# Performance work log

Hardware: AMD Instinct MI355X
Metric: run time of the kernel (lower is better)

Reference implementation:

```python
import jax, jax.numpy as jnp
import numpy as np

# Static config (matches init_kwargs)
B, H, W, C = 8, 80, 60, 512
WS, SHIFT = 10, 5
NH = 16
HD = C // NH  # 32
L = WS * WS  # 100 tokens per window
NW = (H // WS) * (W // WS)  # 48 windows per image
EPS = 1e-5


def _relative_position_index():
    coords = np.stack(np.meshgrid(np.arange(WS), np.arange(WS), indexing='ij'))  # (2,WS,WS)
    flat = coords.reshape(2, -1)  # (2, L)
    rel = flat[:, :, None] - flat[:, None, :]  # (2, L, L)
    rel = rel.transpose(1, 2, 0)  # (L, L, 2)
    rel[:, :, 0] += WS - 1
    rel[:, :, 1] += WS - 1
    rel[:, :, 0] *= 2 * WS - 1
    return rel.sum(-1)  # (L, L) indices into (2*WS-1)^2 table


def _attn_mask():
    # Swin shift mask: label 3x3 regions, tokens in different regions cannot attend.
    img = np.zeros((H, W), dtype=np.float32)
    slices = (slice(0, -WS), slice(-WS, -SHIFT), slice(-SHIFT, None))
    cnt = 0
    for hs in slices:
        for ws_ in slices:
            img[hs, ws_] = cnt
            cnt += 1
    mw = img.reshape(H // WS, WS, W // WS, WS).transpose(0, 2, 1, 3).reshape(NW, L)
    diff = mw[:, None, :] - mw[:, :, None]  # (NW, L, L)
    return np.where(diff != 0, -100.0, 0.0).astype(np.float32)


REL_IDX = jnp.asarray(_relative_position_index())
ATTN_MASK = jnp.asarray(_attn_mask())


def layernorm(x, g, b):
    mu = jnp.mean(x, axis=-1, keepdims=True)
    var = jnp.mean(jnp.square(x - mu), axis=-1, keepdims=True)
    return (x - mu) * jax.lax.rsqrt(var + EPS) * g + b


def setup_inputs() -> dict:
    key = jax.random.key(0)
    ks = jax.random.split(key, 8)
    s = 0.02
    return {
        'hidden_states': jax.random.normal(ks[0], (B, H * W, C), jnp.float32),
        'ln1_g': jnp.ones((C,), jnp.float32),
        'ln1_b': jnp.zeros((C,), jnp.float32),
        'wq': jax.random.normal(ks[1], (C, C), jnp.float32) * s,
        'bq': jnp.zeros((C,), jnp.float32),
        'wk': jax.random.normal(ks[2], (C, C), jnp.float32) * s,
        'bk': jnp.zeros((C,), jnp.float32),
        'wv': jax.random.normal(ks[3], (C, C), jnp.float32) * s,
        'bv': jnp.zeros((C,), jnp.float32),
        'wo': jax.random.normal(ks[4], (C, C), jnp.float32) * s,
        'bo': jnp.zeros((C,), jnp.float32),
        'rel_bias_table': jax.random.normal(ks[5], ((2 * WS - 1) ** 2, NH), jnp.float32) * s,
        'ln2_g': jnp.ones((C,), jnp.float32),
        'ln2_b': jnp.zeros((C,), jnp.float32),
        'w1': jax.random.normal(ks[6], (C, 4 * C), jnp.float32) * s,
        'b1': jnp.zeros((4 * C,), jnp.float32),
        'w2': jax.random.normal(ks[7], (4 * C, C), jnp.float32) * s,
        'b2': jnp.zeros((C,), jnp.float32),
    }


def reference(hidden_states, ln1_g, ln1_b, wq, bq, wk, bk, wv, bv, wo, bo,
              rel_bias_table, ln2_g, ln2_b, w1, b1, w2, b2):
    shortcut = hidden_states  # (B, H*W, C)
    x = layernorm(hidden_states, ln1_g, ln1_b).reshape(B, H, W, C)
    # cyclic shift (H, W divisible by WS -> no padding needed)
    x = jnp.roll(x, (-SHIFT, -SHIFT), axis=(1, 2))
    # window partition -> (B*NW, L, C)
    win = x.reshape(B, H // WS, WS, W // WS, WS, C).transpose(0, 1, 3, 2, 4, 5)
    win = win.reshape(B * NW, L, C)
    # multi-head attention within windows
    q = (win @ wq + bq).reshape(-1, L, NH, HD).transpose(0, 2, 1, 3)
    k = (win @ wk + bk).reshape(-1, L, NH, HD).transpose(0, 2, 1, 3)
    v = (win @ wv + bv).reshape(-1, L, NH, HD).transpose(0, 2, 1, 3)
    scores = jnp.einsum('bhqd,bhkd->bhqk', q, k) / np.sqrt(HD).astype(np.float32)
    bias = rel_bias_table[REL_IDX.reshape(-1)].reshape(L, L, NH).transpose(2, 0, 1)
    scores = scores + bias[None]  # (B*NW, NH, L, L)
    scores = scores.reshape(B, NW, NH, L, L) + ATTN_MASK[None, :, None]
    attn = jax.nn.softmax(scores.reshape(B * NW, NH, L, L), axis=-1)
    ctx = jnp.einsum('bhqk,bhkd->bhqd', attn, v).transpose(0, 2, 1, 3).reshape(B * NW, L, C)
    out = ctx @ wo + bo
    # window reverse + un-shift
    out = out.reshape(B, H // WS, W // WS, WS, WS, C).transpose(0, 1, 3, 2, 4, 5)
    out = out.reshape(B, H, W, C)
    out = jnp.roll(out, (SHIFT, SHIFT), axis=(1, 2)).reshape(B, H * W, C)
    hs = shortcut + out
    # FFN with post-residual layernorm input
    y = layernorm(hs, ln2_g, ln2_b)
    y = jax.nn.gelu(y @ w1 + b1, approximate=False) @ w2 + b2
    return hs + y
```

## Files before the change

kernel.cpp:

```cpp
#include <hip/hip_runtime.h>
#include <math.h>

typedef unsigned short u16;
typedef unsigned int u32;
typedef __bf16 bf16x8 __attribute__((ext_vector_type(8)));
typedef float f32x4 __attribute__((ext_vector_type(4)));

__device__ __forceinline__ float b2f(u16 u) { return __uint_as_float(((u32)u) << 16); }
__device__ __forceinline__ u16 f2b(float f) {
    u32 x = __float_as_uint(f);
    return (u16)((x + 0x7FFFu + ((x >> 16) & 1u)) >> 16);
}
__device__ __forceinline__ void load8f(const float* p, size_t idx, float* o) {
    const float4* q = (const float4*)(p + idx);
    float4 a = q[0], b = q[1];
    o[0]=a.x; o[1]=a.y; o[2]=a.z; o[3]=a.w; o[4]=b.x; o[5]=b.y; o[6]=b.z; o[7]=b.w;
}
__device__ __forceinline__ void gld16(const void* g, void* l) {
    __builtin_amdgcn_global_load_lds(
        (const __attribute__((address_space(1))) u32*)g,
        (__attribute__((address_space(3))) u32*)l, 16, 0, 0);
}

__global__ __launch_bounds__(256) void transpose_k(const float* __restrict__ Win, u16* __restrict__ Wt,
                                                   int Kd, int Nd, float scale) {
    __shared__ u16 tile[32][33];
    int tx = threadIdx.x & 31, ty = threadIdx.x >> 5;
    int k0 = blockIdx.x << 5, n0 = blockIdx.y << 5;
#pragma unroll
    for (int r = 0; r < 4; r++)
        tile[ty + 8 * r][tx] = f2b(Win[(size_t)(k0 + ty + 8 * r) * Nd + (n0 + tx)] * scale);
    __syncthreads();
#pragma unroll
    for (int r = 0; r < 4; r++)
        Wt[(size_t)(n0 + ty + 8 * r) * Kd + (k0 + tx)] = tile[tx][ty + 8 * r];
}

__global__ __launch_bounds__(256) void biascat_k(const float* __restrict__ bq, const float* __restrict__ bk,
                                                 const float* __restrict__ bv, float* __restrict__ o) {
    int i = blockIdx.x * 256 + threadIdx.x;
    float v = (i < 512) ? bq[i] * 0.17677669529663689f : (i < 1024 ? bk[i - 512] : bv[i - 1024]);
    o[i] = v;
}

__global__ __launch_bounds__(256) void ln1win_k(const float* __restrict__ x, const float* __restrict__ g,
                                                const float* __restrict__ bta, u16* __restrict__ win) {
    int wave = threadIdx.x >> 6, lane = threadIdx.x & 63;
    int token = blockIdx.x * 4 + wave;
    int b = token / 4800, rem = token - b * 4800;
    int h = rem / 60, w = rem - h * 60;
    int hr = h + 75; if (hr >= 80) hr -= 80;
    int wr = w + 55; if (wr >= 60) wr -= 60;
    int widx = (hr / 10) * 6 + (wr / 10);
    int l = (hr - (hr / 10) * 10) * 10 + (wr - (wr / 10) * 10);
    size_t dstrow = ((size_t)b * 48 + widx) * 100 + l;
    int c0 = lane * 8;
    float v[8]; load8f(x, (size_t)token * 512 + c0, v);
    float s = 0.f, s2 = 0.f;
#pragma unroll
    for (int e = 0; e < 8; e++) { s += v[e]; s2 += v[e] * v[e]; }
#pragma unroll
    for (int o = 32; o > 0; o >>= 1) { s += __shfl_xor(s, o); s2 += __shfl_xor(s2, o); }
    float mean = s * (1.0f / 512.0f);
    float var = fmaxf(s2 * (1.0f / 512.0f) - mean * mean, 0.0f);
    float rstd = rsqrtf(var + 1e-5f);
    uint4 o4; u16* ou = (u16*)&o4;
#pragma unroll
    for (int e = 0; e < 8; e++)
        ou[e] = f2b((v[e] - mean) * rstd * g[c0 + e] + bta[c0 + e]);
    *(uint4*)(win + dstrow * 512 + c0) = o4;
}

__global__ __launch_bounds__(256) void resid2_k(const float* __restrict__ shortcut, const u16* __restrict__ attn_out,
                                                const float* __restrict__ g, const float* __restrict__ bta,
                                                u16* __restrict__ hs, u16* __restrict__ ln2y) {
    int wave = threadIdx.x >> 6, lane = threadIdx.x & 63;
    int token = blockIdx.x * 4 + wave;
    int b = token / 4800, rem = token - b * 4800;
    int h = rem / 60, w = rem - h * 60;
    int hr = h + 75; if (hr >= 80) hr -= 80;
    int wr = w + 55; if (wr >= 60) wr -= 60;
    int widx = (hr / 10) * 6 + (wr / 10);
    int l = (hr - (hr / 10) * 10) * 10 + (wr - (wr / 10) * 10);
    size_t arow = ((size_t)b * 48 + widx) * 100 + l;
    int c0 = lane * 8;
    float sv[8]; load8f(shortcut, (size_t)token * 512 + c0, sv);
    uint4 da = *(const uint4*)(attn_out + arow * 512 + c0);
    const u16* au = (const u16*)&da;
    float hv[8]; float s = 0.f, s2 = 0.f;
    uint4 oh; u16* ohu = (u16*)&oh;
#pragma unroll
    for (int e = 0; e < 8; e++) {
        hv[e] = sv[e] + b2f(au[e]);
        s += hv[e]; s2 += hv[e] * hv[e];
        ohu[e] = f2b(hv[e]);
    }
    *(uint4*)(hs + (size_t)token * 512 + c0) = oh;
#pragma unroll
    for (int off = 32; off > 0; off >>= 1) { s += __shfl_xor(s, off); s2 += __shfl_xor(s2, off); }
    float mean = s * (1.0f / 512.0f);
    float var = fmaxf(s2 * (1.0f / 512.0f) - mean * mean, 0.0f);
    float rstd = rsqrtf(var + 1e-5f);
    uint4 oy; u16* oyu = (u16*)&oy;
#pragma unroll
    for (int e = 0; e < 8; e++)
        oyu[e] = f2b((hv[e] - mean) * rstd * g[c0 + e] + bta[c0 + e]);
    *(uint4*)(ln2y + (size_t)token * 512 + c0) = oy;
}

template <int EPI, int OF32, int QKV>
__global__ __launch_bounds__(512, 2) void gemm256_k(const u16* __restrict__ A, const u16* __restrict__ Bt,
                                                    const float* __restrict__ bias, const u16* __restrict__ res,
                                                    void* __restrict__ C0, void* __restrict__ C1, void* __restrict__ C2,
                                                    int M, int N, int K) {
    __shared__ __align__(16) u16 As[2][256 * 64];
    __shared__ __align__(16) u16 Bs[2][256 * 64];
    int tid = threadIdx.x;
    int wave = tid >> 6, lane = tid & 63;
    int l15 = lane & 15, quad = lane >> 4;
    int wr = wave >> 2, wc = wave & 3;

    int gy = gridDim.y;
    int nwg = gridDim.x * gy;
    int lid = blockIdx.x + blockIdx.y * gridDim.x;
    int xcd = lid & 7, loc = lid >> 3;
    int q8 = nwg >> 3, r8 = nwg & 7;
    int wg = (xcd < r8 ? xcd * (q8 + 1) : r8 * (q8 + 1) + (xcd - r8) * q8) + loc;
    int bn = wg % gy, bm = wg / gy;

    f32x4 acc[8][4];
#pragma unroll
    for (int i = 0; i < 8; i++)
#pragma unroll
        for (int j = 0; j < 4; j++) acc[i][j] = (f32x4){0.f, 0.f, 0.f, 0.f};

    const u16* Ab = A + (size_t)(bm * 256) * K;
    const u16* Bb = Bt + (size_t)(bn * 256) * K;

    int lrow = lane >> 3;
    int cg = (lane & 7) ^ lrow;
    size_t gOff = (size_t)(wave * 8 + lrow) * K + cg * 8;
    int e = l15 & 7;
    int xk0 = (quad ^ e) * 8;
    int xk1 = xk0 ^ 32;
    int aRow = (wr * 128 + l15) * 64;
    int bRow = (wc * 64 + l15) * 64;

    auto STAGE_A = [&](int b, int kt, int i) {
        gld16(Ab + (size_t)(i * 64) * K + kt + gOff, &As[b][(i * 64 + wave * 8) * 64]);
    };
    auto STAGE_B = [&](int b, int kt, int j) {
        gld16(Bb + (size_t)(j * 64) * K + kt + gOff, &Bs[b][(j * 64 + wave * 8) * 64]);
    };
    auto STAGE8 = [&](int b, int kt) {
        STAGE_B(b, kt, 0); STAGE_B(b, kt, 1); STAGE_B(b, kt, 2); STAGE_B(b, kt, 3);
        STAGE_A(b, kt, 0); STAGE_A(b, kt, 1); STAGE_A(b, kt, 2); STAGE_A(b, kt, 3);
    };

#define MM16(MH)                                                                     \
    do {                                                                             \
        __builtin_amdgcn_s_setprio(1);                                               \
        _Pragma("unroll") for (int i_ = 0; i_ < 4; i_++)                             \
            _Pragma("unroll") for (int n_ = 0; n_ < 4; n_++)                         \
                acc[(MH) * 4 + i_][n_] = __builtin_amdgcn_mfma_f32_16x16x32_bf16(    \
                    a_[i_], b_[n_], acc[(MH) * 4 + i_][n_], 0, 0, 0);                \
        __builtin_amdgcn_s_setprio(0);                                               \
    } while (0)

    int T = K >> 6;
    STAGE8(0, 0);
#pragma unroll 1
    for (int t = 0; t < T; t++) {
        int cur = t & 1, nxt = cur ^ 1;
        if (t + 1 < T) {
            STAGE8(nxt, (t + 1) << 6);
            asm volatile("s_waitcnt vmcnt(8)" ::: "memory");
        } else {
            asm volatile("s_waitcnt vmcnt(0)" ::: "memory");
        }
        __builtin_amdgcn_s_barrier();
        asm volatile("" ::: "memory");
        bf16x8 a_[4], b_[4];
#pragma unroll
        for (int n = 0; n < 4; n++) b_[n] = *(const bf16x8*)(&Bs[cur][bRow + n * 1024 + xk0]);
#pragma unroll
        for (int i = 0; i < 4; i++) a_[i] = *(const bf16x8*)(&As[cur][aRow + i * 1024 + xk0]);
        MM16(0);
#pragma unroll
        for (int i = 0; i < 4; i++) a_[i] = *(const bf16x8*)(&As[cur][aRow + (4 + i) * 1024 + xk0]);
        MM16(1);
#pragma unroll
        for (int n = 0; n < 4; n++) b_[n] = *(const bf16x8*)(&Bs[cur][bRow + n * 1024 + xk1]);
#pragma unroll
        for (int i = 0; i < 4; i++) a_[i] = *(const bf16x8*)(&As[cur][aRow + i * 1024 + xk1]);
        MM16(0);
#pragma unroll
        for (int i = 0; i < 4; i++) a_[i] = *(const bf16x8*)(&As[cur][aRow + (4 + i) * 1024 + xk1]);
        asm volatile("s_waitcnt lgkmcnt(0)" ::: "memory");
        __builtin_amdgcn_sched_barrier(0);
        __builtin_amdgcn_s_barrier();
        asm volatile("" ::: "memory");
        MM16(1);
    }
#undef MM16

    u16* Cd = (u16*)C0;
    if (QKV) {
        int sel = bn >> 1;
        Cd = (sel == 0) ? (u16*)C0 : (sel == 1) ? (u16*)C1 : (u16*)C2;
    }
#pragma unroll
    for (int m = 0; m < 8; m++) {
        int row0 = bm * 256 + wr * 128 + m * 16 + quad * 4;
#pragma unroll
        for (int n = 0; n < 4; n++) {
            int colg = bn * 256 + wc * 64 + n * 16 + l15;
            int col = QKV ? (colg & 511) : colg;
            float bv = bias[colg];
#pragma unroll
            for (int rr = 0; rr < 4; rr++) {
                int row = row0 + rr;
                float v = acc[m][n][rr] + bv;
                if (EPI == 1) {
                    float zz = 1.5957691216f * (v + 0.044715f * v * v * v);
                    float tt = 1.0f - 2.0f / (__expf(zz) + 1.0f);
                    v = 0.5f * v * (1.0f + tt);
                }
                if (EPI == 2) v += b2f(res[(size_t)row * 512 + col]);
                if (OF32) ((float*)Cd)[(size_t)row * N + col] = v;
                else      ((u16*)Cd)[(size_t)row * N + col] = f2b(v);
            }
        }
    }
}

template <int EPI, int OF32>
__global__ __launch_bounds__(256) void gemm128_k(const u16* __restrict__ A, const u16* __restrict__ Bt,
                                                 const float* __restrict__ bias, const u16* __restrict__ res,
                                                 void* __restrict__ C, int M, int N, int K) {
    __shared__ __align__(16) u16 As[3][128 * 32];
    __shared__ __align__(16) u16 Bs[3][128 * 32];
    int tid = threadIdx.x;
    int wave = tid >> 6, lane = tid & 63;
    int l15 = lane & 15, quad = lane >> 4;
    int lq = lane >> 2, lr = lane & 3;
    int wm = (wave >> 1) * 64, wn = (wave & 1) * 64;

    int gy = gridDim.y;
    int nwg = gridDim.x * gy;
    int lid = blockIdx.x + blockIdx.y * gridDim.x;
    int xcd = lid & 7, loc = lid >> 3;
    int q8 = nwg >> 3, r8 = nwg & 7;
    int wg = (xcd < r8 ? xcd * (q8 + 1) : r8 * (q8 + 1) + (xcd - r8) * q8) + loc;
    int bn = wg % gy, bm = wg / gy;

    f32x4 acc[4][4];
#pragma unroll
    for (int i = 0; i < 4; i++)
#pragma unroll
        for (int j = 0; j < 4; j++) acc[i][j] = (f32x4){0.f, 0.f, 0.f, 0.f};

    const u16* Ab = A + (size_t)(bm * 128) * K;
    const u16* Bb = Bt + (size_t)(bn * 128) * K;

    int cgs = (lr ^ (lq & 3)) * 8;
    int xrd = (quad ^ (l15 & 3)) * 8;

    int T = K >> 5;
    auto STAGE = [&](int b, int t) {
        int kt = t << 5;
#pragma unroll
        for (int h = 0; h < 2; h++) {
            int r = h * 64 + wave * 16 + lq;
            gld16(Ab + (size_t)r * K + kt + cgs, &As[b][(h * 64 + wave * 16) * 32]);
            gld16(Bb + (size_t)r * K + kt + cgs, &Bs[b][(h * 64 + wave * 16) * 32]);
        }
    };

    STAGE(0, 0);
    STAGE(1, 1);
    for (int t = 0; t < T; t++) {
        int cb = t % 3;
        if (t + 2 < T) STAGE((t + 2) % 3, t + 2);
        if (t + 2 < T)      asm volatile("s_waitcnt vmcnt(8)" ::: "memory");
        else if (t + 1 < T) asm volatile("s_waitcnt vmcnt(4)" ::: "memory");
        else                asm volatile("s_waitcnt vmcnt(0)" ::: "memory");
        __builtin_amdgcn_s_barrier();
        asm volatile("" ::: "memory");
        bf16x8 af[4], bfr[4];
#pragma unroll
        for (int x = 0; x < 4; x++) {
            af[x]  = *(const bf16x8*)(&As[cb][(wm + x * 16 + l15) * 32 + xrd]);
            bfr[x] = *(const bf16x8*)(&Bs[cb][(wn + x * 16 + l15) * 32 + xrd]);
        }
        asm volatile("s_waitcnt lgkmcnt(0)" ::: "memory");
        __builtin_amdgcn_sched_barrier(0);
        __builtin_amdgcn_s_barrier();
        asm volatile("" ::: "memory");
#pragma unroll
        for (int i = 0; i < 4; i++)
#pragma unroll
            for (int j = 0; j < 4; j++)
                acc[i][j] = __builtin_amdgcn_mfma_f32_16x16x32_bf16(af[i], bfr[j], acc[i][j], 0, 0, 0);
    }

    u16* Cd = (u16*)C;
#pragma unroll
    for (int i = 0; i < 4; i++) {
        int row0 = bm * 128 + wm + i * 16 + quad * 4;
#pragma unroll
        for (int j = 0; j < 4; j++) {
            int col = bn * 128 + wn + j * 16 + l15;
            float bv = bias[col];
#pragma unroll
            for (int rr = 0; rr < 4; rr++) {
                int row = row0 + rr;
                float v = acc[i][j][rr] + bv;
                if (EPI == 1) {
                    float zz = 1.5957691216f * (v + 0.044715f * v * v * v);
                    float tt = 1.0f - 2.0f / (__expf(zz) + 1.0f);
                    v = 0.5f * v * (1.0f + tt);
                }
                if (EPI == 2) v += b2f(res[(size_t)row * 512 + col]);
                if (OF32) ((float*)Cd)[(size_t)row * N + col] = v;
                else      ((u16*)Cd)[(size_t)row * N + col] = f2b(v);
            }
        }
    }
}

__global__ __launch_bounds__(256) void biasprep_k(const float* __restrict__ table, u16* __restrict__ biasM) {
    int idx = blockIdx.x * 256 + threadIdx.x;
    int k = idx % 112;
    int t = idx / 112;
    int q = t % 100; t /= 100;
    int head = t & 15, wt = t >> 4;
    float v;
    if (k >= 100) {
        v = -1e30f;
    } else {
        int qi = q / 10, qj = q - qi * 10;
        int ki = k / 10, kj = k - ki * 10;
        int rel = (qi - ki) * 19 + (qj - kj) + 180;
        v = table[rel * 16 + head];
        int rq = ((wt & 2) ? (qi < 5 ? 4 : 8) : 0) + ((wt & 1) ? (qj < 5 ? 1 : 2) : 0);
        int rk = ((wt & 2) ? (ki < 5 ? 4 : 8) : 0) + ((wt & 1) ? (kj < 5 ? 1 : 2) : 0);
        if (rq != rk) v -= 100.0f;
    }
    biasM[idx] = f2b(v);
}

__global__ __launch_bounds__(256, 3) void attn_mfma_k(const u16* __restrict__ Q, const u16* __restrict__ Km,
                                                      const u16* __restrict__ V, const u16* __restrict__ biasM,
                                                      u16* __restrict__ ctx) {
    __shared__ __align__(16) u16 lds[4 * 6144];
    int tid = threadIdx.x;
    int wave = tid >> 6, lane = tid & 63;
    int l15 = lane & 15, quad = lane >> 4;
    int bid = blockIdx.x;
    int win = bid >> 2;
    int head = ((bid & 3) << 2) + wave;
    int w48 = win % 48;
    int wh = w48 / 6, ww = w48 - wh * 6;
    int wtype = ((wh == 7) ? 2 : 0) + ((ww == 5) ? 1 : 0);
    size_t base = (size_t)win * 51200 + head * 32;
    u16* Vt = lds + wave * 6144;
    u16* Pl = Vt + 4096;
    const u16* bptr = biasM + (size_t)(wtype * 16 + head) * 11200;

    {
        uint4 z = {0u, 0u, 0u, 0u};
#pragma unroll
        for (int r = 0; r < 2; r++) {
            int c = r * 64 + lane;
            int d = c >> 2, seg = c & 3;
            int k0 = 96 + seg * 8;
            *(uint4*)(Vt + d * 128 + (k0 ^ ((d & 7) << 3))) = z;
        }
        uint2 z2 = {0u, 0u};
        *(uint2*)(Pl + l15 * 128 + ((112 + quad * 4) ^ ((l15 & 7) << 3))) = z2;
    }
#pragma unroll
    for (int r = 0; r < 2; r++) {
        int k = r * 64 + lane;
        if (k < 100) {
            const uint4* vp = (const uint4*)(V + base + (size_t)k * 512);
#pragma unroll
            for (int c = 0; c < 4; c++) {
                uint4 dv = vp[c];
                const u16* e = (const u16*)&dv;
#pragma unroll
                for (int t = 0; t < 8; t++) {
                    int d = c * 8 + t;
                    Vt[d * 128 + (k ^ ((d & 7) << 3))] = e[t];
                }
            }
        }
    }
    bf16x8 kf[7];
#pragma unroll
    for (int i = 0; i < 7; i++) {
        int kr = i * 16 + l15; if (kr > 99) kr = 99;
        kf[i] = *(const bf16x8*)(Km + base + (size_t)kr * 512 + quad * 8);
    }
    bf16x8 vf[2][4];
#pragma unroll
    for (int it = 0; it < 2; it++)
#pragma unroll
        for (int ks = 0; ks < 4; ks++) {
            int D = it * 16 + l15;
            vf[it][ks] = *(const bf16x8*)(Vt + D * 128 + ((ks * 32 + quad * 8) ^ ((D & 7) << 3)));
        }

#pragma unroll 1
    for (int j = 0; j < 7; j++) {
        int q = j * 16 + l15;
        int qc = q > 99 ? 99 : q;
        bf16x8 qf = *(const bf16x8*)(Q + base + (size_t)qc * 512 + quad * 8);
        f32x4 s[7];
#pragma unroll
        for (int i = 0; i < 7; i++) {
            uint2 bb = *(const uint2*)(bptr + (size_t)qc * 112 + i * 16 + quad * 4);
            const u16* be = (const u16*)&bb;
            s[i][0] = b2f(be[0]); s[i][1] = b2f(be[1]);
            s[i][2] = b2f(be[2]); s[i][3] = b2f(be[3]);
        }
#pragma unroll
        for (int i = 0; i < 7; i++)
            s[i] = __builtin_amdgcn_mfma_f32_16x16x32_bf16(kf[i], qf, s[i], 0, 0, 0);
        float m = -1e30f;
#pragma unroll
        for (int i = 0; i < 7; i++)
#pragma unroll
            for (int rr = 0; rr < 4; rr++) m = fmaxf(m, s[i][rr]);
        m = fmaxf(m, __shfl_xor(m, 16));
        m = fmaxf(m, __shfl_xor(m, 32));
        float l = 0.f;
#pragma unroll
        for (int i = 0; i < 7; i++)
#pragma unroll
            for (int rr = 0; rr < 4; rr++) { s[i][rr] = __expf(s[i][rr] - m); l += s[i][rr]; }
        l += __shfl_xor(l, 16);
        l += __shfl_xor(l, 32);
#pragma unroll
        for (int i = 0; i < 7; i++) {
            u32 lo, hi;
            asm("v_cvt_pk_bf16_f32 %0, %1, %2" : "=v"(lo) : "v"(s[i][0]), "v"(s[i][1]));
            asm("v_cvt_pk_bf16_f32 %0, %1, %2" : "=v"(hi) : "v"(s[i][2]), "v"(s[i][3]));
            uint2 w; w.x = lo; w.y = hi;
            *(uint2*)(Pl + l15 * 128 + ((i * 16 + quad * 4) ^ ((l15 & 7) << 3))) = w;
        }
        f32x4 o0 = (f32x4){0.f, 0.f, 0.f, 0.f};
        f32x4 o1 = (f32x4){0.f, 0.f, 0.f, 0.f};
#pragma unroll
        for (int ks = 0; ks < 4; ks++) {
            bf16x8 pf = *(const bf16x8*)(Pl + l15 * 128 + ((ks * 32 + quad * 8) ^ ((l15 & 7) << 3)));
            o0 = __builtin_amdgcn_mfma_f32_16x16x32_bf16(vf[0][ks], pf, o0, 0, 0, 0);
            o1 = __builtin_amdgcn_mfma_f32_16x16x32_bf16(vf[1][ks], pf, o1, 0, 0, 0);
        }
        float inv = 1.0f / l;
        if (q < 100) {
            u16* cp = ctx + base + (size_t)q * 512;
            {
                float a0 = o0[0]*inv, a1 = o0[1]*inv, a2 = o0[2]*inv, a3 = o0[3]*inv;
                u32 lo, hi;
                asm("v_cvt_pk_bf16_f32 %0, %1, %2" : "=v"(lo) : "v"(a0), "v"(a1));
                asm("v_cvt_pk_bf16_f32 %0, %1, %2" : "=v"(hi) : "v"(a2), "v"(a3));
                uint2 w; w.x = lo; w.y = hi;
                *(uint2*)(cp + quad * 4) = w;
            }
            {
                float a0 = o1[0]*inv, a1 = o1[1]*inv, a2 = o1[2]*inv, a3 = o1[3]*inv;
                u32 lo, hi;
                asm("v_cvt_pk_bf16_f32 %0, %1, %2" : "=v"(lo) : "v"(a0), "v"(a1));
                asm("v_cvt_pk_bf16_f32 %0, %1, %2" : "=v"(hi) : "v"(a2), "v"(a3));
                uint2 w; w.x = lo; w.y = hi;
                *(uint2*)(cp + 16 + quad * 4) = w;
            }
        }
    }
}

extern "C" void kernel_launch(void* const* d_in, const int* in_sizes, int n_in,
                              void* d_out, int out_size, void* d_ws, size_t ws_size,
                              hipStream_t stream) {
    const float* hidden = (const float*)d_in[0];
    const float* ln1_g  = (const float*)d_in[1];
    const float* ln1_b  = (const float*)d_in[2];
    const float* wq = (const float*)d_in[3];  const float* bq = (const float*)d_in[4];
    const float* wk = (const float*)d_in[5];  const float* bk = (const float*)d_in[6];
    const float* wv = (const float*)d_in[7];  const float* bv = (const float*)d_in[8];
    const float* wo = (const float*)d_in[9];  const float* bo = (const float*)d_in[10];
    const float* rel = (const float*)d_in[11];
    const float* ln2_g = (const float*)d_in[12];
    const float* ln2_b = (const float*)d_in[13];
    const float* w1 = (const float*)d_in[14]; const float* b1 = (const float*)d_in[15];
    const float* w2 = (const float*)d_in[16]; const float* b2 = (const float*)d_in[17];

    const size_t NTC = 38400ull * 512;
    u16* ws = (u16*)d_ws;
    u16* R0 = ws;
    u16* R1 = ws + NTC;
    u16* Rh = ws + 2 * NTC;
    u16* wqt = ws + 3 * NTC;
    u16* wkt = wqt + 512 * 512;
    u16* wvt = wkt + 512 * 512;
    u16* wot = wvt + 512 * 512;
    u16* w1t = wot + 512 * 512;
    u16* w2t = w1t + 1048576;
    float* qkvb = (float*)(w2t + 1048576);
    u16* dlo = (u16*)d_out;
    u16* biasM = dlo + NTC;
    float* outp = (float*)d_out;

    const float SC = 0.17677669529663689f;

    transpose_k<<<dim3(16, 16), 256, 0, stream>>>(wq, wqt, 512, 512, SC);
    transpose_k<<<dim3(16, 16), 256, 0, stream>>>(wk, wkt, 512, 512, 1.0f);
    transpose_k<<<dim3(16, 16), 256, 0, stream>>>(wv, wvt, 512, 512, 1.0f);
    transpose_k<<<dim3(16, 16), 256, 0, stream>>>(wo, wot, 512, 512, 1.0f);
    transpose_k<<<dim3(16, 64), 256, 0, stream>>>(w1, w1t, 512, 2048, 1.0f);
    transpose_k<<<dim3(64, 16), 256, 0, stream>>>(w2, w2t, 2048, 512, 1.0f);
    biascat_k<<<6, 256, 0, stream>>>(bq, bk, bv, qkvb);
    biasprep_k<<<2800, 256, 0, stream>>>(rel, biasM);

    ln1win_k<<<9600, 256, 0, stream>>>(hidden, ln1_g, ln1_b, R0 );

    gemm256_k<0, 0, 1><<<dim3(150, 6), 512, 0, stream>>>(R0, wqt, qkvb, nullptr,
                                                         R1 , Rh , dlo , 38400, 512, 512);

    attn_mfma_k<<<1536, 256, 0, stream>>>(R1, Rh, dlo, biasM, R0 );

    gemm128_k<0, 0><<<dim3(300, 4), 256, 0, stream>>>(R0, wot, bo, nullptr,
                                                      R1 , 38400, 512, 512);

    resid2_k<<<9600, 256, 0, stream>>>(hidden, R1, ln2_g, ln2_b, Rh , dlo );

    for (int mc = 1; mc >= 0; mc--) {
        size_t roff = (size_t)mc * 19200 * 512;
        gemm256_k<1, 0, 0><<<dim3(75, 8), 512, 0, stream>>>(dlo + roff, w1t, b1, nullptr,
                                                            R0 , nullptr, nullptr, 19200, 2048, 512);
        gemm128_k<2, 1><<<dim3(150, 4), 256, 0, stream>>>(R0, w2t, b2, Rh + roff,
                                                          outp + roff, 19200, 512, 2048);
    }
}
```

Measured before the change: 729.5 us.

## Rework 128x128 GEMM to K=64 double-buffered tiles with split MFMA phases

Replaces the triple-buffered K=32 gemm128 kernel with a double-buffered K=64 variant that uses a new XOR-swizzled LDS layout. Each iteration is split into two MFMA half-steps, so the second half's LDS reads overlap the first half's math, and MFMAs run at raised wave priority. It also adds a launch bound asking for two blocks per CU. The aim is to halve barrier count per K, improve LDS/compute overlap and raise occupancy for the output projection and FFN down GEMMs. The cost is less prefetch depth, and register pressure could limit the two-block occupancy target.

```diff
diff --git a/kernel.cpp b/kernel.cpp
--- a/kernel.cpp
+++ b/kernel.cpp
@@ -235,16 +235,15 @@
 }
 
 template <int EPI, int OF32>
-__global__ __launch_bounds__(256) void gemm128_k(const u16* __restrict__ A, const u16* __restrict__ Bt,
-                                                 const float* __restrict__ bias, const u16* __restrict__ res,
-                                                 void* __restrict__ C, int M, int N, int K) {
-    __shared__ __align__(16) u16 As[3][128 * 32];
-    __shared__ __align__(16) u16 Bs[3][128 * 32];
+__global__ __launch_bounds__(256, 2) void gemmB_k(const u16* __restrict__ A, const u16* __restrict__ Bt,
+                                                  const float* __restrict__ bias, const u16* __restrict__ res,
+                                                  void* __restrict__ C, int M, int N, int K) {
+    __shared__ __align__(16) u16 As[2][128 * 64];
+    __shared__ __align__(16) u16 Bs[2][128 * 64];
     int tid = threadIdx.x;
     int wave = tid >> 6, lane = tid & 63;
     int l15 = lane & 15, quad = lane >> 4;
-    int lq = lane >> 2, lr = lane & 3;
-    int wm = (wave >> 1) * 64, wn = (wave & 1) * 64;
+    int wr = wave >> 1, wc = wave & 1;
 
     int gy = gridDim.y;
     int nwg = gridDim.x * gy;
@@ -263,54 +262,74 @@
     const u16* Ab = A + (size_t)(bm * 128) * K;
     const u16* Bb = Bt + (size_t)(bn * 128) * K;
 
-    int cgs = (lr ^ (lq & 3)) * 8;
-    int xrd = (quad ^ (l15 & 3)) * 8;
-
-    int T = K >> 5;
-    auto STAGE = [&](int b, int t) {
-        int kt = t << 5;
-#pragma unroll
-        for (int h = 0; h < 2; h++) {
-            int r = h * 64 + wave * 16 + lq;
-            gld16(Ab + (size_t)r * K + kt + cgs, &As[b][(h * 64 + wave * 16) * 32]);
-            gld16(Bb + (size_t)r * K + kt + cgs, &Bs[b][(h * 64 + wave * 16) * 32]);
-        }
+    int lrow = lane >> 3;
+    int cg = (lane & 7) ^ lrow;
+    size_t gOff = (size_t)(wave * 8 + lrow) * K + cg * 8;
+    int e = l15 & 7;
+    int xk0 = (quad ^ e) * 8;
+    int xk1 = xk0 ^ 32;
+    int aRow = (wr * 64 + l15) * 64;
+    int bRow = (wc * 64 + l15) * 64;
+
+    auto STAGE_A = [&](int b, int kt, int i) {
+        gld16(Ab + (size_t)(i * 32) * K + kt + gOff, &As[b][(i * 32 + wave * 8) * 64]);
     };
-
-    STAGE(0, 0);
-    STAGE(1, 1);
+    auto STAGE_B = [&](int b, int kt, int j) {
+        gld16(Bb + (size_t)(j * 32) * K + kt + gOff, &Bs[b][(j * 32 + wave * 8) * 64]);
+    };
+    auto STAGE8 = [&](int b, int kt) {
+        STAGE_B(b, kt, 0); STAGE_B(b, kt, 1); STAGE_B(b, kt, 2); STAGE_B(b, kt, 3);
+        STAGE_A(b, kt, 0); STAGE_A(b, kt, 1); STAGE_A(b, kt, 2); STAGE_A(b, kt, 3);
+    };
+
+#define MMALL()                                                                      \
+    do {                                                                             \
+        __builtin_amdgcn_s_setprio(1);                                               \
+        _Pragma("unroll") for (int i_ = 0; i_ < 4; i_++)                             \
+            _Pragma("unroll") for (int n_ = 0; n_ < 4; n_++)                         \
+                acc[i_][n_] = __builtin_amdgcn_mfma_f32_16x16x32_bf16(               \
+                    a_[i_], b_[n_], acc[i_][n_], 0, 0, 0);                           \
+        __builtin_amdgcn_s_setprio(0);                                               \
+    } while (0)
+
+    int T = K >> 6;
+    STAGE8(0, 0);
+#pragma unroll 1
     for (int t = 0; t < T; t++) {
-        int cb = t % 3;
-        if (t + 2 < T) STAGE((t + 2) % 3, t + 2);
-        if (t + 2 < T)      asm volatile("s_waitcnt vmcnt(8)" ::: "memory");
-        else if (t + 1 < T) asm volatile("s_waitcnt vmcnt(4)" ::: "memory");
-        else                asm volatile("s_waitcnt vmcnt(0)" ::: "memory");
+        int cur = t & 1, nxt = cur ^ 1;
+        if (t + 1 < T) {
+            STAGE8(nxt, (t + 1) << 6);
+            asm volatile("s_waitcnt vmcnt(8)" ::: "memory");
+        } else {
+            asm volatile("s_waitcnt vmcnt(0)" ::: "memory");
+        }
         __builtin_amdgcn_s_barrier();
         asm volatile("" ::: "memory");
-        bf16x8 af[4], bfr[4];
-#pragma unroll
-        for (int x = 0; x < 4; x++) {
-            af[x]  = *(const bf16x8*)(&As[cb][(wm + x * 16 + l15) * 32 + xrd]);
-            bfr[x] = *(const bf16x8*)(&Bs[cb][(wn + x * 16 + l15) * 32 + xrd]);
-        }
+        bf16x8 a_[4], b_[4];
+#pragma unroll
+        for (int n = 0; n < 4; n++) b_[n] = *(const bf16x8*)(&Bs[cur][bRow + n * 1024 + xk0]);
+#pragma unroll
+        for (int i = 0; i < 4; i++) a_[i] = *(const bf16x8*)(&As[cur][aRow + i * 1024 + xk0]);
+        MMALL();
+#pragma unroll
+        for (int n = 0; n < 4; n++) b_[n] = *(const bf16x8*)(&Bs[cur][bRow + n * 1024 + xk1]);
+#pragma unroll
+        for (int i = 0; i < 4; i++) a_[i] = *(const bf16x8*)(&As[cur][aRow + i * 1024 + xk1]);
         asm volatile("s_waitcnt lgkmcnt(0)" ::: "memory");
         __builtin_amdgcn_sched_barrier(0);
         __builtin_amdgcn_s_barrier();
         asm volatile("" ::: "memory");
-#pragma unroll
-        for (int i = 0; i < 4; i++)
-#pragma unroll
-            for (int j = 0; j < 4; j++)
-                acc[i][j] = __builtin_amdgcn_mfma_f32_16x16x32_bf16(af[i], bfr[j], acc[i][j], 0, 0, 0);
-    }
+        MMALL();
+    }
+#undef MMALL
 
     u16* Cd = (u16*)C;
 #pragma unroll
     for (int i = 0; i < 4; i++) {
-        int row0 = bm * 128 + wm + i * 16 + quad * 4;
+        int row0 = bm * 128 + wr * 64 + i * 16 + quad * 4;
 #pragma unroll
         for (int j = 0; j < 4; j++) {
-            int col = bn * 128 + wn + j * 16 + l15;
+            int col = bn * 128 + wc * 64 + j * 16 + l15;
             float bv = bias[col];
 #pragma unroll
             for (int rr = 0; rr < 4; rr++) {
@@ -531,8 +550,8 @@
 
     attn_mfma_k<<<1536, 256, 0, stream>>>(R1, Rh, dlo, biasM, R0 );
 
-    gemm128_k<0, 0><<<dim3(300, 4), 256, 0, stream>>>(R0, wot, bo, nullptr,
-                                                      R1 , 38400, 512, 512);
+    gemmB_k<0, 0><<<dim3(300, 4), 256, 0, stream>>>(R0, wot, bo, nullptr,
+                                                    R1 , 38400, 512, 512);
 
     resid2_k<<<9600, 256, 0, stream>>>(hidden, R1, ln2_g, ln2_b, Rh , dlo );
 
@@ -540,7 +559,7 @@
         size_t roff = (size_t)mc * 19200 * 512;
         gemm256_k<1, 0, 0><<<dim3(75, 8), 512, 0, stream>>>(dlo + roff, w1t, b1, nullptr,
                                                             R0 , nullptr, nullptr, 19200, 2048, 512);
-        gemm128_k<2, 1><<<dim3(150, 4), 256, 0, stream>>>(R0, w2t, b2, Rh + roff,
-                                                          outp + roff, 19200, 512, 2048);
-    }
-}
+        gemmB_k<2, 1><<<dim3(150, 4), 256, 0, stream>>>(R0, w2t, b2, Rh + roff,
+                                                        outp + roff, 19200, 512, 2048);
+    }
+}
```

New measurement: 685.0 us. 6.1% less time.
